# Optimization experiments

Measured on AMD Instinct MI355X. Metric: run time of the kernel, lower is better.

Reference implementation:

```python
import jax, jax.numpy as jnp
import numpy as np


def setup_inputs() -> dict:
    key = jax.random.key(0)
    k1, k2 = jax.random.split(key)
    D = 512
    B, N = 32, 512
    panel_embeddings = jax.random.normal(k1, (B, N, D), dtype=jnp.float32)
    # nn.Bilinear(D, D, 1) weight: (1, D, D) -> squeeze to (D, D); bias: scalar
    bound = 1.0 / np.sqrt(D)
    W = jax.random.uniform(k2, (D, D), dtype=jnp.float32, minval=-bound, maxval=bound)
    b = jnp.float32(0.0)
    return {"panel_embeddings": panel_embeddings, "W": W, "b": b}


def reference(panel_embeddings, W, b):
    # score[b,i,j] = x_i^T W x_j + b, with diagonal forced to 0 (loop skips i==j)
    xw = jnp.einsum('bid,de->bie', panel_embeddings, W)          # (B, N, D)
    scores = jnp.einsum('bie,bje->bij', xw, panel_embeddings) + b  # (B, N, N)
    N = panel_embeddings.shape[1]
    mask = ~jnp.eye(N, dtype=bool)
    return jnp.where(mask, scores, jnp.zeros_like(scores))
```

## Files before the change

kernel.cpp:

```cpp
#include <hip/hip_runtime.h>
#include <stdint.h>

#define BATCH 32
#define NDIM 512
#define DDIM 512
#define XELEMS (BATCH * NDIM * DDIM)

typedef _Float16 f16x8 __attribute__((ext_vector_type(8)));
typedef float f32x4 __attribute__((ext_vector_type(4)));

__device__ __forceinline__ f16x8 cvt8(float4 u0, float4 u1) {
    f16x8 r;
    r[0] = (_Float16)u0.x; r[1] = (_Float16)u0.y;
    r[2] = (_Float16)u0.z; r[3] = (_Float16)u0.w;
    r[4] = (_Float16)u1.x; r[5] = (_Float16)u1.y;
    r[6] = (_Float16)u1.z; r[7] = (_Float16)u1.w;
    return r;
}

__device__ __forceinline__ void gl_lds16(const _Float16* g, _Float16* l) {
    __builtin_amdgcn_global_load_lds(
        (const __attribute__((address_space(1))) unsigned int*)(g),
        (__attribute__((address_space(3))) unsigned int*)(l),
        16, 0, 0);
}

#define WAITVM(N) do { asm volatile("s_waitcnt vmcnt(" #N ")" ::: "memory"); \
                       __builtin_amdgcn_sched_barrier(0); } while (0)


__global__ __launch_bounds__(256) void prep(const float* __restrict__ X,
                                            _Float16* __restrict__ XhT,
                                            const float* __restrict__ W,
                                            _Float16* __restrict__ WtT) {
    int bid = blockIdx.x;
    if (bid < 4096) {
        int g    = bid * 4 + (threadIdx.x >> 6);
        int lane = threadIdx.x & 63;
        int b  = g >> 9;
        int kt = (g >> 5) & 15;
        int ch = g & 31;
        int r = lane >> 2, s = lane & 3;
        int col = kt * 32 + ((s ^ ((r >> 1) & 3)) << 3);
        const float* src = X + ((size_t)(b * 512 + ch * 16 + r)) * DDIM + col;
        float4 u0 = *(const float4*)src;
        float4 u1 = *(const float4*)(src + 4);
        *(f16x8*)&XhT[(size_t)g * 512 + lane * 8] = cvt8(u0, u1);
    } else {
        __shared__ float tile[32][33];
        int t  = bid - 4096;
        int bx = t & 15;
        int by = t >> 4;
        int tx = threadIdx.x & 31;
        int ty = threadIdx.x >> 5;
        for (int rr = ty; rr < 32; rr += 8)
            tile[rr][tx] = W[(by * 32 + rr) * DDIM + bx * 32 + tx];
        __syncthreads();
        int idx = threadIdx.x;
        if (idx < 128) {
            int er = idx >> 2;
            int sp = idx & 3;
            int rr = er & 15;
            int sl = sp ^ ((rr >> 1) & 3);
            f16x8 v;
#pragma unroll
            for (int j = 0; j < 8; ++j)
                v[j] = (_Float16)tile[sl * 8 + j][er];
            int ch = bx * 2 + (er >> 4);
            *(f16x8*)&WtT[((size_t)(by * 32 + ch)) * 512 + rr * 32 + sp * 8] = v;
        }
    }
}

__global__ __launch_bounds__(512) void fused(const _Float16* __restrict__ XhT,
                                             const _Float16* __restrict__ WtT,
                                             float* __restrict__ Sout,
                                             const float* __restrict__ bias_ptr) {
    __shared__ __align__(16) _Float16 AY[64 * 512];
    __shared__ __align__(16) _Float16 Bs[2][8 * 2048];

    const int tid  = threadIdx.x;
    const int lane = tid & 63;
    const int wv   = tid >> 6;
    const int quad = lane >> 4;
    const int l16  = lane & 15;
    const int l8   = lane * 8;

    const int paK = (quad ^ ((l16 >> 1) & 3)) * 8;

    const int blk   = blockIdx.x;
    const int batch = blk & 31;
    const int r0    = (blk >> 5) * 64;
    const int ch0   = r0 >> 4;

    const _Float16* Xt = XhT + (size_t)(batch * 16) * 32 * 512;

    f32x4 acc[4][4];
#pragma unroll
    for (int i = 0; i < 4; ++i)
#pragma unroll
        for (int j = 0; j < 4; ++j)
            acc[i][j] = (f32x4){0.f, 0.f, 0.f, 0.f};

#pragma unroll
    for (int c = 0; c < 8; ++c) {
        const int kt = wv * 2 + (c >> 2);
        const int rc = c & 3;
        gl_lds16(Xt + ((size_t)(kt * 32 + ch0 + rc)) * 512 + l8,
                 &AY[(kt * 4 + rc) * 512]);
    }
#pragma unroll
    for (int t = 0; t < 4; ++t)
        gl_lds16(WtT + ((size_t)(0 * 32 + wv * 4 + t)) * 512 + l8,
                 &Bs[0][wv * 2048 + t * 512]);
    WAITVM(4);
    __builtin_amdgcn_s_barrier();

#pragma unroll
    for (int it = 0; it < 15; ++it) {
        const int buf = it & 1;
        const int ktn = it + 1;
#pragma unroll
        for (int t = 0; t < 4; ++t)
            gl_lds16(WtT + ((size_t)(ktn * 32 + wv * 4 + t)) * 512 + l8,
                     &Bs[buf ^ 1][wv * 2048 + t * 512]);
        WAITVM(4);
        f16x8 a[4], b[4];
#pragma unroll
        for (int mt = 0; mt < 4; ++mt)
            a[mt] = *(const f16x8*)&AY[(it * 4 + mt) * 512 + l16 * 32 + paK];
#pragma unroll
        for (int nt = 0; nt < 4; ++nt)
            b[nt] = *(const f16x8*)&Bs[buf][wv * 2048 + nt * 512 + l16 * 32 + paK];
#pragma unroll
        for (int mt = 0; mt < 4; ++mt)
#pragma unroll
            for (int nt = 0; nt < 4; ++nt)
                acc[mt][nt] = __builtin_amdgcn_mfma_f32_16x16x32_f16(
                    a[mt], b[nt], acc[mt][nt], 0, 0, 0);
    }
    {
        const int buf = 15 & 1;
#pragma unroll
        for (int t = 0; t < 4; ++t)
            gl_lds16(Xt + ((size_t)(0 * 32 + wv * 4 + t)) * 512 + l8,
                     &Bs[buf ^ 1][wv * 2048 + t * 512]);
        WAITVM(4);
        f16x8 a[4], b[4];
#pragma unroll
        for (int mt = 0; mt < 4; ++mt)
            a[mt] = *(const f16x8*)&AY[(15 * 4 + mt) * 512 + l16 * 32 + paK];
#pragma unroll
        for (int nt = 0; nt < 4; ++nt)
            b[nt] = *(const f16x8*)&Bs[buf][wv * 2048 + nt * 512 + l16 * 32 + paK];
#pragma unroll
        for (int mt = 0; mt < 4; ++mt)
#pragma unroll
            for (int nt = 0; nt < 4; ++nt)
                acc[mt][nt] = __builtin_amdgcn_mfma_f32_16x16x32_f16(
                    a[mt], b[nt], acc[mt][nt], 0, 0, 0);
    }

    __builtin_amdgcn_s_barrier();
#pragma unroll
    for (int mt = 0; mt < 4; ++mt)
#pragma unroll
        for (int nt = 0; nt < 4; ++nt)
#pragma unroll
            for (int r = 0; r < 4; ++r) {
                int i = mt * 16 + quad * 4 + r;
                int e = wv * 64 + nt * 16 + l16;
                int c = e >> 3, j = e & 7;
                AY[i * 512 + (((c ^ (i & 7)) << 3) | j)] = (_Float16)acc[mt][nt][r];
            }
    asm volatile("s_waitcnt lgkmcnt(0)" ::: "memory");
    __builtin_amdgcn_s_barrier();

#pragma unroll
    for (int i = 0; i < 4; ++i)
#pragma unroll
        for (int j = 0; j < 4; ++j)
            acc[i][j] = (f32x4){0.f, 0.f, 0.f, 0.f};

#pragma unroll
    for (int it = 0; it < 15; ++it) {
        const int buf = it & 1;
        const int etn = it + 1;
#pragma unroll
        for (int t = 0; t < 4; ++t)
            gl_lds16(Xt + ((size_t)(etn * 32 + wv * 4 + t)) * 512 + l8,
                     &Bs[buf ^ 1][wv * 2048 + t * 512]);
        WAITVM(4);
        const int pay = (((it * 4 + quad) ^ (l16 & 7)) * 8);
        f16x8 a[4], b[4];
#pragma unroll
        for (int mt = 0; mt < 4; ++mt)
            a[mt] = *(const f16x8*)&AY[(mt * 16 + l16) * 512 + pay];
#pragma unroll
        for (int nt = 0; nt < 4; ++nt)
            b[nt] = *(const f16x8*)&Bs[buf][wv * 2048 + nt * 512 + l16 * 32 + paK];
#pragma unroll
        for (int mt = 0; mt < 4; ++mt)
#pragma unroll
            for (int nt = 0; nt < 4; ++nt)
                acc[mt][nt] = __builtin_amdgcn_mfma_f32_16x16x32_f16(
                    a[mt], b[nt], acc[mt][nt], 0, 0, 0);
    }
    {
        const int buf = 15 & 1;
        WAITVM(0);
        const int pay = (((15 * 4 + quad) ^ (l16 & 7)) * 8);
        f16x8 a[4], b[4];
#pragma unroll
        for (int mt = 0; mt < 4; ++mt)
            a[mt] = *(const f16x8*)&AY[(mt * 16 + l16) * 512 + pay];
#pragma unroll
        for (int nt = 0; nt < 4; ++nt)
            b[nt] = *(const f16x8*)&Bs[buf][wv * 2048 + nt * 512 + l16 * 32 + paK];
#pragma unroll
        for (int mt = 0; mt < 4; ++mt)
#pragma unroll
            for (int nt = 0; nt < 4; ++nt)
                acc[mt][nt] = __builtin_amdgcn_mfma_f32_16x16x32_f16(
                    a[mt], b[nt], acc[mt][nt], 0, 0, 0);
    }

    const float bias = bias_ptr[0];
#pragma unroll
    for (int mt = 0; mt < 4; ++mt)
#pragma unroll
        for (int nt = 0; nt < 4; ++nt)
#pragma unroll
            for (int r = 0; r < 4; ++r) {
                int gi = r0 + mt * 16 + quad * 4 + r;
                int gj = wv * 64 + nt * 16 + l16;
                float v = acc[mt][nt][r] + bias;
                if (gi == gj) v = 0.f;
                Sout[((size_t)batch * NDIM + gi) * NDIM + gj] = v;
            }
}

extern "C" void kernel_launch(void* const* d_in, const int* in_sizes, int n_in,
                              void* d_out, int out_size, void* d_ws, size_t ws_size,
                              hipStream_t stream) {
    const float* X  = (const float*)d_in[0];
    const float* W  = (const float*)d_in[1];
    const float* bp = (const float*)d_in[2];
    float* out = (float*)d_out;

    _Float16* XhT = (_Float16*)d_ws;
    _Float16* WtT = XhT + XELEMS;

    prep<<<4096 + 256, 256, 0, stream>>>(X, XhT, W, WtT);

    fused<<<256, 512, 0, stream>>>(XhT, WtT, out, bp);

    (void)in_sizes; (void)n_in; (void)out_size; (void)ws_size;
}
```

Before: 107.0 us.

## Load B operands directly from global into registers and halve LDS footprint

Drops the global_load_lds double-buffered LDS staging for the W and X B-operands. Each wave now loads its private B fragments straight from global memory into registers, prefetching two k-steps ahead. The A tile keeps its LDS staging, now filled with ordinary vector loads and a barrier. Removing the Bs buffer cuts LDS to 64 KB, which together with launch_bounds(512,2) aims for two blocks per CU. The cost is more register pressure, and each wave's fragment loads from global are less coalesced.

```diff
diff --git a/kernel.cpp b/kernel.cpp
--- a/kernel.cpp
+++ b/kernel.cpp
@@ -17,16 +17,6 @@
     r[6] = (_Float16)u1.z; r[7] = (_Float16)u1.w;
     return r;
 }
-
-__device__ __forceinline__ void gl_lds16(const _Float16* g, _Float16* l) {
-    __builtin_amdgcn_global_load_lds(
-        (const __attribute__((address_space(1))) unsigned int*)(g),
-        (__attribute__((address_space(3))) unsigned int*)(l),
-        16, 0, 0);
-}
-
-#define WAITVM(N) do { asm volatile("s_waitcnt vmcnt(" #N ")" ::: "memory"); \
-                       __builtin_amdgcn_sched_barrier(0); } while (0)
 
 
 __global__ __launch_bounds__(256) void prep(const float* __restrict__ X,
@@ -72,21 +62,20 @@
     }
 }
 
-__global__ __launch_bounds__(512) void fused(const _Float16* __restrict__ XhT,
-                                             const _Float16* __restrict__ WtT,
-                                             float* __restrict__ Sout,
-                                             const float* __restrict__ bias_ptr) {
+__global__ __launch_bounds__(512, 2) void fused(const _Float16* __restrict__ XhT,
+                                                const _Float16* __restrict__ WtT,
+                                                float* __restrict__ Sout,
+                                                const float* __restrict__ bias_ptr) {
     __shared__ __align__(16) _Float16 AY[64 * 512];
-    __shared__ __align__(16) _Float16 Bs[2][8 * 2048];
 
     const int tid  = threadIdx.x;
     const int lane = tid & 63;
     const int wv   = tid >> 6;
     const int quad = lane >> 4;
     const int l16  = lane & 15;
-    const int l8   = lane * 8;
 
     const int paK = (quad ^ ((l16 >> 1) & 3)) * 8;
+    const int fro = l16 * 32 + paK;
 
     const int blk   = blockIdx.x;
     const int batch = blk & 31;
@@ -106,62 +95,43 @@
     for (int c = 0; c < 8; ++c) {
         const int kt = wv * 2 + (c >> 2);
         const int rc = c & 3;
-        gl_lds16(Xt + ((size_t)(kt * 32 + ch0 + rc)) * 512 + l8,
-                 &AY[(kt * 4 + rc) * 512]);
-    }
-#pragma unroll
-    for (int t = 0; t < 4; ++t)
-        gl_lds16(WtT + ((size_t)(0 * 32 + wv * 4 + t)) * 512 + l8,
-                 &Bs[0][wv * 2048 + t * 512]);
-    WAITVM(4);
-    __builtin_amdgcn_s_barrier();
-
-#pragma unroll
-    for (int it = 0; it < 15; ++it) {
-        const int buf = it & 1;
-        const int ktn = it + 1;
-#pragma unroll
-        for (int t = 0; t < 4; ++t)
-            gl_lds16(WtT + ((size_t)(ktn * 32 + wv * 4 + t)) * 512 + l8,
-                     &Bs[buf ^ 1][wv * 2048 + t * 512]);
-        WAITVM(4);
-        f16x8 a[4], b[4];
-#pragma unroll
-        for (int mt = 0; mt < 4; ++mt)
-            a[mt] = *(const f16x8*)&AY[(it * 4 + mt) * 512 + l16 * 32 + paK];
-#pragma unroll
-        for (int nt = 0; nt < 4; ++nt)
-            b[nt] = *(const f16x8*)&Bs[buf][wv * 2048 + nt * 512 + l16 * 32 + paK];
+        f16x8 v = *(const f16x8*)&Xt[((size_t)(kt * 32 + ch0 + rc)) * 512 + lane * 8];
+        *(f16x8*)&AY[(kt * 4 + rc) * 512 + lane * 8] = v;
+    }
+    __syncthreads();
+
+    f16x8 bb[2][4];
+#pragma unroll
+    for (int d = 0; d < 2; ++d)
+#pragma unroll
+        for (int nt = 0; nt < 4; ++nt)
+            bb[d][nt] = *(const f16x8*)&WtT[((size_t)(d * 32 + wv * 4 + nt)) * 512 + fro];
+
+#pragma unroll
+    for (int it = 0; it < 16; ++it) {
+        const int s = it & 1;
+        f16x8 bcur[4];
+#pragma unroll
+        for (int nt = 0; nt < 4; ++nt)
+            bcur[nt] = bb[s][nt];
+        if (it + 2 < 16) {
+#pragma unroll
+            for (int nt = 0; nt < 4; ++nt)
+                bb[s][nt] = *(const f16x8*)&WtT[((size_t)((it + 2) * 32 + wv * 4 + nt)) * 512 + fro];
+        }
+        f16x8 a[4];
+#pragma unroll
+        for (int mt = 0; mt < 4; ++mt)
+            a[mt] = *(const f16x8*)&AY[(it * 4 + mt) * 512 + fro];
 #pragma unroll
         for (int mt = 0; mt < 4; ++mt)
 #pragma unroll
             for (int nt = 0; nt < 4; ++nt)
                 acc[mt][nt] = __builtin_amdgcn_mfma_f32_16x16x32_f16(
-                    a[mt], b[nt], acc[mt][nt], 0, 0, 0);
-    }
-    {
-        const int buf = 15 & 1;
-#pragma unroll
-        for (int t = 0; t < 4; ++t)
-            gl_lds16(Xt + ((size_t)(0 * 32 + wv * 4 + t)) * 512 + l8,
-                     &Bs[buf ^ 1][wv * 2048 + t * 512]);
-        WAITVM(4);
-        f16x8 a[4], b[4];
-#pragma unroll
-        for (int mt = 0; mt < 4; ++mt)
-            a[mt] = *(const f16x8*)&AY[(15 * 4 + mt) * 512 + l16 * 32 + paK];
-#pragma unroll
-        for (int nt = 0; nt < 4; ++nt)
-            b[nt] = *(const f16x8*)&Bs[buf][wv * 2048 + nt * 512 + l16 * 32 + paK];
-#pragma unroll
-        for (int mt = 0; mt < 4; ++mt)
-#pragma unroll
-            for (int nt = 0; nt < 4; ++nt)
-                acc[mt][nt] = __builtin_amdgcn_mfma_f32_16x16x32_f16(
-                    a[mt], b[nt], acc[mt][nt], 0, 0, 0);
-    }
-
-    __builtin_amdgcn_s_barrier();
+                    a[mt], bcur[nt], acc[mt][nt], 0, 0, 0);
+    }
+
+    __syncthreads();
 #pragma unroll
     for (int mt = 0; mt < 4; ++mt)
 #pragma unroll
@@ -173,8 +143,7 @@
                 int c = e >> 3, j = e & 7;
                 AY[i * 512 + (((c ^ (i & 7)) << 3) | j)] = (_Float16)acc[mt][nt][r];
             }
-    asm volatile("s_waitcnt lgkmcnt(0)" ::: "memory");
-    __builtin_amdgcn_s_barrier();
+    __syncthreads();
 
 #pragma unroll
     for (int i = 0; i < 4; ++i)
@@ -182,47 +151,36 @@
         for (int j = 0; j < 4; ++j)
             acc[i][j] = (f32x4){0.f, 0.f, 0.f, 0.f};
 
-#pragma unroll
-    for (int it = 0; it < 15; ++it) {
-        const int buf = it & 1;
-        const int etn = it + 1;
-#pragma unroll
-        for (int t = 0; t < 4; ++t)
-            gl_lds16(Xt + ((size_t)(etn * 32 + wv * 4 + t)) * 512 + l8,
-                     &Bs[buf ^ 1][wv * 2048 + t * 512]);
-        WAITVM(4);
+    f16x8 cb[2][4];
+#pragma unroll
+    for (int d = 0; d < 2; ++d)
+#pragma unroll
+        for (int nt = 0; nt < 4; ++nt)
+            cb[d][nt] = *(const f16x8*)&Xt[((size_t)(d * 32 + wv * 4 + nt)) * 512 + fro];
+
+#pragma unroll
+    for (int it = 0; it < 16; ++it) {
+        const int s = it & 1;
+        f16x8 bcur[4];
+#pragma unroll
+        for (int nt = 0; nt < 4; ++nt)
+            bcur[nt] = cb[s][nt];
+        if (it + 2 < 16) {
+#pragma unroll
+            for (int nt = 0; nt < 4; ++nt)
+                cb[s][nt] = *(const f16x8*)&Xt[((size_t)((it + 2) * 32 + wv * 4 + nt)) * 512 + fro];
+        }
         const int pay = (((it * 4 + quad) ^ (l16 & 7)) * 8);
-        f16x8 a[4], b[4];
+        f16x8 a[4];
 #pragma unroll
         for (int mt = 0; mt < 4; ++mt)
             a[mt] = *(const f16x8*)&AY[(mt * 16 + l16) * 512 + pay];
 #pragma unroll
-        for (int nt = 0; nt < 4; ++nt)
-            b[nt] = *(const f16x8*)&Bs[buf][wv * 2048 + nt * 512 + l16 * 32 + paK];
-#pragma unroll
         for (int mt = 0; mt < 4; ++mt)
 #pragma unroll
             for (int nt = 0; nt < 4; ++nt)
                 acc[mt][nt] = __builtin_amdgcn_mfma_f32_16x16x32_f16(
-                    a[mt], b[nt], acc[mt][nt], 0, 0, 0);
-    }
-    {
-        const int buf = 15 & 1;
-        WAITVM(0);
-        const int pay = (((15 * 4 + quad) ^ (l16 & 7)) * 8);
-        f16x8 a[4], b[4];
-#pragma unroll
-        for (int mt = 0; mt < 4; ++mt)
-            a[mt] = *(const f16x8*)&AY[(mt * 16 + l16) * 512 + pay];
-#pragma unroll
-        for (int nt = 0; nt < 4; ++nt)
-            b[nt] = *(const f16x8*)&Bs[buf][wv * 2048 + nt * 512 + l16 * 32 + paK];
-#pragma unroll
-        for (int mt = 0; mt < 4; ++mt)
-#pragma unroll
-            for (int nt = 0; nt < 4; ++nt)
-                acc[mt][nt] = __builtin_amdgcn_mfma_f32_16x16x32_f16(
-                    a[mt], b[nt], acc[mt][nt], 0, 0, 0);
+                    a[mt], bcur[nt], acc[mt][nt], 0, 0, 0);
     }
 
     const float bias = bias_ptr[0];
```

New measurement: 105.8 us. No clear change (-1.1%).

## Merge prep and GEMM kernels into one cooperative launch with grid sync

Applied to the files above, without the earlier changes.

Folds the fp32-to-fp16 conversion and swizzle of X and the transpose of W into the main fused kernel. The 256 blocks do the prep work first, then meet at a grid-wide barrier, and the kernel is launched with hipLaunchCooperativeKernel. This removes the second kernel launch and its inter-kernel gap. In exchange, the conversion now runs on only 256 blocks of 512 threads at low occupancy, and a grid sync plus threadfence is added.

```diff
diff --git a/kernel.cpp b/kernel.cpp
--- a/kernel.cpp
+++ b/kernel.cpp
@@ -1,5 +1,8 @@
 #include <hip/hip_runtime.h>
+#include <hip/hip_cooperative_groups.h>
 #include <stdint.h>
+
+namespace cg = cooperative_groups;
 
 #define BATCH 32
 #define NDIM 512
@@ -29,53 +32,12 @@
                        __builtin_amdgcn_sched_barrier(0); } while (0)
 
 
-__global__ __launch_bounds__(256) void prep(const float* __restrict__ X,
-                                            _Float16* __restrict__ XhT,
-                                            const float* __restrict__ W,
-                                            _Float16* __restrict__ WtT) {
-    int bid = blockIdx.x;
-    if (bid < 4096) {
-        int g    = bid * 4 + (threadIdx.x >> 6);
-        int lane = threadIdx.x & 63;
-        int b  = g >> 9;
-        int kt = (g >> 5) & 15;
-        int ch = g & 31;
-        int r = lane >> 2, s = lane & 3;
-        int col = kt * 32 + ((s ^ ((r >> 1) & 3)) << 3);
-        const float* src = X + ((size_t)(b * 512 + ch * 16 + r)) * DDIM + col;
-        float4 u0 = *(const float4*)src;
-        float4 u1 = *(const float4*)(src + 4);
-        *(f16x8*)&XhT[(size_t)g * 512 + lane * 8] = cvt8(u0, u1);
-    } else {
-        __shared__ float tile[32][33];
-        int t  = bid - 4096;
-        int bx = t & 15;
-        int by = t >> 4;
-        int tx = threadIdx.x & 31;
-        int ty = threadIdx.x >> 5;
-        for (int rr = ty; rr < 32; rr += 8)
-            tile[rr][tx] = W[(by * 32 + rr) * DDIM + bx * 32 + tx];
-        __syncthreads();
-        int idx = threadIdx.x;
-        if (idx < 128) {
-            int er = idx >> 2;
-            int sp = idx & 3;
-            int rr = er & 15;
-            int sl = sp ^ ((rr >> 1) & 3);
-            f16x8 v;
-#pragma unroll
-            for (int j = 0; j < 8; ++j)
-                v[j] = (_Float16)tile[sl * 8 + j][er];
-            int ch = bx * 2 + (er >> 4);
-            *(f16x8*)&WtT[((size_t)(by * 32 + ch)) * 512 + rr * 32 + sp * 8] = v;
-        }
-    }
-}
-
-__global__ __launch_bounds__(512) void fused(const _Float16* __restrict__ XhT,
-                                             const _Float16* __restrict__ WtT,
-                                             float* __restrict__ Sout,
-                                             const float* __restrict__ bias_ptr) {
+__global__ __launch_bounds__(512) void fused_all(const float* __restrict__ X,
+                                                 _Float16* __restrict__ XhT,
+                                                 const float* __restrict__ W,
+                                                 _Float16* __restrict__ WtT,
+                                                 float* __restrict__ Sout,
+                                                 const float* __restrict__ bias_ptr) {
     __shared__ __align__(16) _Float16 AY[64 * 512];
     __shared__ __align__(16) _Float16 Bs[2][8 * 2048];
 
@@ -85,10 +47,51 @@
     const int quad = lane >> 4;
     const int l16  = lane & 15;
     const int l8   = lane * 8;
+    const int blk  = blockIdx.x;
+
+    {
+        const int r = lane >> 2, s = lane & 3;
+#pragma unroll
+        for (int i = 0; i < 8; ++i) {
+            const int g  = blk * 64 + wv * 8 + i;
+            const int b  = g >> 9;
+            const int kt = (g >> 5) & 15;
+            const int ch = g & 31;
+            const int col = kt * 32 + ((s ^ ((r >> 1) & 3)) << 3);
+            const float* src = X + ((size_t)(b * 512 + ch * 16 + r)) * DDIM + col;
+            float4 u0 = *(const float4*)src;
+            float4 u1 = *(const float4*)(src + 4);
+            *(f16x8*)&XhT[(size_t)g * 512 + lane * 8] = cvt8(u0, u1);
+        }
+
+        float* tileF = (float*)&AY[0];
+        const int bx = blk & 15;
+        const int by = blk >> 4;
+        if (tid < 256) {
+            const int tx = tid & 31;
+            const int ty = tid >> 5;
+            for (int rr = ty; rr < 32; rr += 8)
+                tileF[rr * 33 + tx] = W[(by * 32 + rr) * DDIM + bx * 32 + tx];
+        }
+        __syncthreads();
+        if (tid < 128) {
+            const int er = tid >> 2;
+            const int sp = tid & 3;
+            const int rr = er & 15;
+            const int sl = sp ^ ((rr >> 1) & 3);
+            f16x8 v;
+#pragma unroll
+            for (int j = 0; j < 8; ++j)
+                v[j] = (_Float16)tileF[(sl * 8 + j) * 33 + er];
+            const int ch = bx * 2 + (er >> 4);
+            *(f16x8*)&WtT[((size_t)(by * 32 + ch)) * 512 + rr * 32 + sp * 8] = v;
+        }
+    }
+
+    __threadfence();
+    cg::this_grid().sync();
 
     const int paK = (quad ^ ((l16 >> 1) & 3)) * 8;
-
-    const int blk   = blockIdx.x;
     const int batch = blk & 31;
     const int r0    = (blk >> 5) * 64;
     const int ch0   = r0 >> 4;
@@ -251,9 +254,8 @@
     _Float16* XhT = (_Float16*)d_ws;
     _Float16* WtT = XhT + XELEMS;
 
-    prep<<<4096 + 256, 256, 0, stream>>>(X, XhT, W, WtT);
-
-    fused<<<256, 512, 0, stream>>>(XhT, WtT, out, bp);
-
-    (void)in_sizes; (void)n_in; (void)out_size; (void)ws_size;
-}
+    void* args[] = { (void*)&X, (void*)&XhT, (void*)&W, (void*)&WtT,
+                     (void*)&out, (void*)&bp };
+    hipLaunchCooperativeKernel((const void*)fused_all, dim3(256), dim3(512),
+                               args, 0, stream);
+}
```

Result: slower. 213.7 us (+99.8%).
